# Performance work log

Hardware: AMD Instinct MI355X
Metric: run time of the kernel (lower is better)

## Reference

```python
import jax, jax.numpy as jnp
import numpy as np

B, K, L, D, H, A = 32, 512, 6, 2048, 16, 10
HD = D // H
OBS = 128
MAX_STEPS = 512


def _ln(x, g, b, eps=1e-5):
    m = x.mean(-1, keepdims=True)
    v = ((x - m) ** 2).mean(-1, keepdims=True)
    return (x - m) * jax.lax.rsqrt(v + eps) * g + b


def _pos_encoding(seq_len, dim):
    # torch: seq counts down from seq_len-1 to 0
    seq = jnp.arange(seq_len - 1, -1, -1, dtype=jnp.float32)
    inv = 10000.0 ** (-(jnp.arange(0, dim, 2, dtype=jnp.float32)) / dim)
    si = seq[:, None] * inv[None, :]
    return jnp.concatenate([jnp.sin(si), jnp.cos(si)], axis=-1)  # [seq_len, dim]


def setup_inputs() -> dict:
    key = jax.random.key(0)
    ks = jax.random.split(key, 16)
    s = 0.02
    inp = {}
    inp['x'] = jax.random.normal(ks[0], (B, OBS), jnp.float32)
    inp['memories'] = jax.random.normal(ks[1], (B, K, L, D), jnp.float32)
    inp['mask'] = jax.random.randint(ks[2], (B, K), 0, 2, jnp.int32)
    inp['memory_indices'] = jax.random.randint(ks[3], (B, K), 0, MAX_STEPS, jnp.int32)
    # encoder (vector-obs Linear)
    inp['enc_w'] = jax.random.normal(ks[4], (D, OBS), jnp.float32) * s
    inp['enc_b'] = jnp.zeros((D,), jnp.float32)
    # per-layer params, stacked on leading L axis
    inp['lnq_g'] = jnp.ones((L, D), jnp.float32)
    inp['lnq_b'] = jnp.zeros((L, D), jnp.float32)
    inp['lnkv_g'] = jnp.ones((L, D), jnp.float32)
    inp['lnkv_b'] = jnp.zeros((L, D), jnp.float32)
    inp['lnattn_g'] = jnp.ones((L, D), jnp.float32)
    inp['lnattn_b'] = jnp.zeros((L, D), jnp.float32)
    inp['wq'] = jax.random.normal(ks[5], (L, HD, HD), jnp.float32) * s
    inp['wk'] = jax.random.normal(ks[6], (L, HD, HD), jnp.float32) * s
    inp['wv'] = jax.random.normal(ks[7], (L, HD, HD), jnp.float32) * s
    inp['wo'] = jax.random.normal(ks[8], (L, D, D), jnp.float32) * s
    inp['bo'] = jnp.zeros((L, D), jnp.float32)
    inp['fc_w'] = jax.random.normal(ks[9], (L, D, D), jnp.float32) * s
    inp['fc_b'] = jnp.zeros((L, D), jnp.float32)
    # heads
    inp['post_w'] = jax.random.normal(ks[10], (D, D), jnp.float32) * s
    inp['post_b'] = jnp.zeros((D,), jnp.float32)
    inp['actor_w'] = jax.random.normal(ks[11], (A, D), jnp.float32) * 0.01
    inp['actor_b'] = jnp.zeros((A,), jnp.float32)
    inp['critic_w'] = jax.random.normal(ks[12], (1, D), jnp.float32) * s
    inp['critic_b'] = jnp.zeros((1,), jnp.float32)
    return inp


def reference(x, memories, mask, memory_indices, enc_w, enc_b,
              lnq_g, lnq_b, lnkv_g, lnkv_b, lnattn_g, lnattn_b,
              wq, wk, wv, wo, bo, fc_w, fc_b,
              post_w, post_b, actor_w, actor_b, critic_w, critic_b):
    h = x @ enc_w.T + enc_b                              # [B, D] encoder
    pe = _pos_encoding(MAX_STEPS, D)[memory_indices]      # [B, K, D]
    mems = memories + pe[:, :, None, :]                   # [B, K, L, D]
    mems_t = jnp.moveaxis(mems, 2, 0)                     # [L, B, K, D]
    maskf = mask[:, None, :] != 0                         # [B, 1, K] -> bcast over heads
    inv_scale = 1.0 / jnp.sqrt(jnp.float32(D))            # note: full embed_dim, as in source

    def body(xq, p):
        lg, lb, kg, kb, ag, ab, Wq, Wk, Wv, Wo, bo_, Fw, Fb, mem = p
        q_ = _ln(xq, lg, lb)                              # [B, D] (query LN)
        kv = _ln(mem, kg, kb)                             # [B, K, D] (key = value = LN(mem))
        q = jnp.einsum('bhd,ed->bhe', q_.reshape(B, H, HD), Wq)
        k = jnp.einsum('bkhd,ed->bkhe', kv.reshape(B, K, H, HD), Wk)
        v = jnp.einsum('bkhd,ed->bkhe', kv.reshape(B, K, H, HD), Wv)
        energy = jnp.einsum('bhd,bkhd->bhk', q, k)        # [B, H, K]
        energy = jnp.where(maskf, energy, jnp.float32(-1e20))
        attn = jax.nn.softmax(energy * inv_scale, axis=-1)
        o = jnp.einsum('bhk,bkhd->bhd', attn, v).reshape(B, D)
        o = o @ Wo.T + bo_                                # fc_out
        xr = o + xq                                       # residual
        f = jax.nn.relu(_ln(xr, ag, ab) @ Fw.T + Fb)      # LN + MLP
        return f + xr, None

    h, _ = jax.lax.scan(
        body, h,
        (lnq_g, lnq_b, lnkv_g, lnkv_b, lnattn_g, lnattn_b,
         wq, wk, wv, wo, bo, fc_w, fc_b, mems_t))

    hid = jax.nn.relu(h @ post_w.T + post_b)
    logits = hid @ actor_w.T + actor_b                    # [B, A]
    value = hid @ critic_w.T + critic_b                   # [B, 1]
    return jnp.concatenate([logits, value], axis=-1)      # [B, A+1]
```

## Files before the change

kernel.cpp:

```cpp
#include <hip/hip_runtime.h>
#include <math.h>

namespace {

constexpr int B_ = 32, K_ = 512, L_ = 6, D_ = 2048, H_ = 16, HD_ = 128;
constexpr int OBS_ = 128, MAXS_ = 512, A_ = 10;
constexpr int NCH = 64, WKEYS = 8;
constexpr int KSPLIT = 8, KCHUNK = 256;
constexpr float EPS = 1e-5f;
constexpr float INV_SCALE = 0.022097086912079608f;

__device__ __forceinline__ float wsum64(float v) {
  v += __shfl_xor(v, 32); v += __shfl_xor(v, 16); v += __shfl_xor(v, 8);
  v += __shfl_xor(v, 4);  v += __shfl_xor(v, 2);  v += __shfl_xor(v, 1);
  return v;
}

__global__ __launch_bounds__(256) void k_pe(float* __restrict__ pe) {
  int s = blockIdx.x, t = threadIdx.x;
  float seqv = (float)(MAXS_ - 1 - s);
  const float c = 13.287712379549449f / 1024.0f;
  for (int r = 0; r < 8; ++r) {
    int j = t + 256 * r;
    int i = (j < 1024) ? j : j - 1024;
    float inv = exp2f(-c * (float)i);
    float a = seqv * inv;
    pe[(size_t)s * D_ + j] = (j < 1024) ? sinf(a) : cosf(a);
  }
}

__global__ __launch_bounds__(128) void k_enc(const float* __restrict__ x,
                                             const float* __restrict__ ew,
                                             const float* __restrict__ eb,
                                             float* __restrict__ h) {
  int b = blockIdx.x, et = blockIdx.y, t = threadIdx.x;
  __shared__ float xs[OBS_];
  xs[t] = x[b * OBS_ + t];
  __syncthreads();
  int e = et * 128 + t;
  const float* wr = ew + (size_t)e * OBS_;
  float acc = eb[e];
  for (int o = 0; o < OBS_; ++o) acc += xs[o] * wr[o];
  h[(size_t)b * D_ + e] = acc;
}

__global__ __launch_bounds__(256) void k_qw(const float* __restrict__ h,
                                            const float* __restrict__ g,
                                            const float* __restrict__ bvec,
                                            const float* __restrict__ Wq,
                                            const float* __restrict__ Wk,
                                            float* __restrict__ qW) {
  int b = blockIdx.x, t = threadIdx.x;
  int lane = t & 63, wv = t >> 6;
  __shared__ float qn[D_];
  __shared__ float qs[D_];
  __shared__ float rs[4], rq[4];
  float4 v0 = *(const float4*)(h + (size_t)b * D_ + t * 8);
  float4 v1 = *(const float4*)(h + (size_t)b * D_ + t * 8 + 4);
  float ls = v0.x + v0.y + v0.z + v0.w + v1.x + v1.y + v1.z + v1.w;
  float lq = v0.x * v0.x + v0.y * v0.y + v0.z * v0.z + v0.w * v0.w +
             v1.x * v1.x + v1.y * v1.y + v1.z * v1.z + v1.w * v1.w;
  ls = wsum64(ls); lq = wsum64(lq);
  if (lane == 0) { rs[wv] = ls; rq[wv] = lq; }
  __syncthreads();
  float sum = rs[0] + rs[1] + rs[2] + rs[3];
  float sq  = rq[0] + rq[1] + rq[2] + rq[3];
  float mean = sum * (1.f / D_);
  float rstd = rsqrtf(sq * (1.f / D_) - mean * mean + EPS);
  {
    float4 g0 = *(const float4*)(g + t * 8);
    float4 g1 = *(const float4*)(g + t * 8 + 4);
    float4 b0 = *(const float4*)(bvec + t * 8);
    float4 b1 = *(const float4*)(bvec + t * 8 + 4);
    qn[t * 8 + 0] = (v0.x - mean) * rstd * g0.x + b0.x;
    qn[t * 8 + 1] = (v0.y - mean) * rstd * g0.y + b0.y;
    qn[t * 8 + 2] = (v0.z - mean) * rstd * g0.z + b0.z;
    qn[t * 8 + 3] = (v0.w - mean) * rstd * g0.w + b0.w;
    qn[t * 8 + 4] = (v1.x - mean) * rstd * g1.x + b1.x;
    qn[t * 8 + 5] = (v1.y - mean) * rstd * g1.y + b1.y;
    qn[t * 8 + 6] = (v1.z - mean) * rstd * g1.z + b1.z;
    qn[t * 8 + 7] = (v1.w - mean) * rstd * g1.w + b1.w;
  }
  __syncthreads();
  int qid = t >> 4;
  int li = t & 15;
  for (int e = 0; e < 128; ++e) {
    const float4* wr = (const float4*)(Wq + (size_t)e * HD_ + li * 8);
    const float4* qv = (const float4*)(qn + qid * HD_ + li * 8);
    float4 w0 = wr[0], w1 = wr[1], a0 = qv[0], a1 = qv[1];
    float acc = w0.x * a0.x + w0.y * a0.y + w0.z * a0.z + w0.w * a0.w +
                w1.x * a1.x + w1.y * a1.y + w1.z * a1.z + w1.w * a1.w;
    acc += __shfl_xor(acc, 1); acc += __shfl_xor(acc, 2);
    acc += __shfl_xor(acc, 4); acc += __shfl_xor(acc, 8);
    if (li == 0) qs[qid * HD_ + e] = acc;
  }
  __syncthreads();
  for (int r = 0; r < 8; ++r) {
    int j = t + 256 * r;
    int hh = j >> 7, d = j & 127;
    const float* qv = qs + hh * HD_;
    float acc = 0.f;
    for (int e = 0; e < HD_; ++e) acc += qv[e] * Wk[(size_t)e * HD_ + d];
    qW[(size_t)b * D_ + j] = acc * INV_SCALE;
  }
}

__global__ __launch_bounds__(256) void k_attn(const float* __restrict__ mem,
                                              const float* __restrict__ pe,
                                              const int* __restrict__ mask,
                                              const int* __restrict__ midx,
                                              const float* __restrict__ g,
                                              const float* __restrict__ bvec,
                                              const float* __restrict__ qW,
                                              float* __restrict__ pm,
                                              float* __restrict__ ps,
                                              float* __restrict__ pctx,
                                              int layer) {
  int b = blockIdx.x;
  int t = threadIdx.x;
  int wid = t >> 6, l = t & 63;
  int ch = blockIdx.y * 4 + wid;
  int hi = l >> 5;
  int ll = l & 31;

  __shared__ float gs[D_], bs[D_], qs[D_];
  for (int i = t; i < D_ / 4; i += 256) {
    ((float4*)gs)[i] = ((const float4*)g)[i];
    ((float4*)bs)[i] = ((const float4*)bvec)[i];
    ((float4*)qs)[i] = ((const float4*)(qW + (size_t)b * D_))[i];
  }
  __syncthreads();

  float m[8], s[8];
  float4 ctx[8];
  #pragma unroll
  for (int i = 0; i < 8; ++i) {
    m[i] = -INFINITY; s[i] = 0.f; ctx[i] = {0.f, 0.f, 0.f, 0.f};
  }

  const size_t browbase = ((size_t)b * K_) * (L_ * D_) + (size_t)layer * D_;
  int kk0 = ch * WKEYS;
  for (int kk = kk0; kk < kk0 + WKEYS; ++kk) {
    if (mask[b * K_ + kk] == 0) continue;
    int pidx = midx[b * K_ + kk];
    const float4* mp = (const float4*)(mem + browbase + (size_t)kk * (L_ * D_));
    const float4* pp = (const float4*)(pe + (size_t)pidx * D_);
    float4 x[8];
    #pragma unroll
    for (int i = 0; i < 8; ++i) {
      float4 a = mp[i * 64 + l];
      float4 c = pp[i * 64 + l];
      x[i] = {a.x + c.x, a.y + c.y, a.z + c.z, a.w + c.w};
    }
    float ls = 0.f, lq = 0.f;
    #pragma unroll
    for (int i = 0; i < 8; ++i) {
      ls += x[i].x + x[i].y + x[i].z + x[i].w;
      lq += x[i].x * x[i].x + x[i].y * x[i].y + x[i].z * x[i].z + x[i].w * x[i].w;
    }
    ls = wsum64(ls); lq = wsum64(lq);
    float mean = ls * (1.f / D_);
    float rstd = rsqrtf(lq * (1.f / D_) - mean * mean + EPS);
    #pragma unroll
    for (int i = 0; i < 8; ++i) {
      int idx = i * 64 + l;
      float4 g4 = ((const float4*)gs)[idx];
      float4 b4 = ((const float4*)bs)[idx];
      float4 q4 = ((const float4*)qs)[idx];
      float4 kv;
      kv.x = (x[i].x - mean) * rstd * g4.x + b4.x;
      kv.y = (x[i].y - mean) * rstd * g4.y + b4.y;
      kv.z = (x[i].z - mean) * rstd * g4.z + b4.z;
      kv.w = (x[i].w - mean) * rstd * g4.w + b4.w;
      float p = kv.x * q4.x + kv.y * q4.y + kv.z * q4.z + kv.w * q4.w;
      p += __shfl_xor(p, 1); p += __shfl_xor(p, 2); p += __shfl_xor(p, 4);
      p += __shfl_xor(p, 8); p += __shfl_xor(p, 16);
      float mn = fmaxf(m[i], p);
      float sc = __expf(m[i] - mn);
      float w = __expf(p - mn);
      s[i] = s[i] * sc + w;
      ctx[i].x = ctx[i].x * sc + w * kv.x;
      ctx[i].y = ctx[i].y * sc + w * kv.y;
      ctx[i].z = ctx[i].z * sc + w * kv.z;
      ctx[i].w = ctx[i].w * sc + w * kv.w;
      m[i] = mn;
    }
  }

  #pragma unroll
  for (int i = 0; i < 8; ++i) {
    int head = 2 * i + hi;
    size_t base = (size_t)(b * H_ + head) * NCH + ch;
    *(float4*)(pctx + base * HD_ + 4 * ll) = ctx[i];
    if (ll == 0) { pm[base] = m[i]; ps[base] = s[i]; }
  }
}

__global__ __launch_bounds__(128) void k_reduce(const float* __restrict__ pm,
                                                const float* __restrict__ ps,
                                                const float* __restrict__ pctx,
                                                const float* __restrict__ Wv,
                                                float* __restrict__ opre) {
  int hh = blockIdx.x, b = blockIdx.y;
  int t = threadIdx.x;
  size_t base = (size_t)(b * H_ + hh) * NCH;
  float m = -INFINITY;
  for (int c = 0; c < NCH; ++c) m = fmaxf(m, pm[base + c]);
  float stot = 0.f, acc = 0.f;
  for (int c = 0; c < NCH; ++c) {
    float wc = __expf(pm[base + c] - m);
    stot += ps[base + c] * wc;
    acc += pctx[(base + c) * HD_ + t] * wc;
  }
  float ctxn = (stot > 0.f) ? acc / stot : 0.f;
  __shared__ float cs[HD_];
  cs[t] = ctxn;
  __syncthreads();
  const float* wr = Wv + (size_t)t * HD_;
  float o = 0.f;
  for (int d = 0; d < HD_; ++d) o += wr[d] * cs[d];
  opre[(size_t)b * D_ + hh * HD_ + t] = o;
}

__global__ __launch_bounds__(256) void k_mv(const float* __restrict__ X,
                                            const float* __restrict__ W,
                                            float* __restrict__ part) {
  int et = blockIdx.x, kc = blockIdx.y;
  int t = threadIdx.x;
  __shared__ float xs[32][260];
  for (int r = 0; r < 8; ++r) {
    int i = t + 256 * r;
    int b = i >> 6, j = i & 63;
    float4 v = *(const float4*)(X + (size_t)b * D_ + kc * KCHUNK + 4 * j);
    *(float4*)(&xs[b][4 * j]) = v;
  }
  __syncthreads();
  int b = t & 31, eg = t >> 5;
  const float* wbase = W + (size_t)(et * 64 + eg * 8) * D_ + kc * KCHUNK;
  float acc[8] = {0.f, 0.f, 0.f, 0.f, 0.f, 0.f, 0.f, 0.f};
  for (int j = 0; j < 64; ++j) {
    float4 x4 = *(const float4*)(&xs[b][4 * j]);
    #pragma unroll
    for (int i = 0; i < 8; ++i) {
      float4 w4 = *(const float4*)(wbase + (size_t)i * D_ + 4 * j);
      acc[i] += w4.x * x4.x + w4.y * x4.y + w4.z * x4.z + w4.w * x4.w;
    }
  }
  float* pb = part + ((size_t)b * KSPLIT + kc) * D_ + et * 64 + eg * 8;
  float4 o0 = {acc[0], acc[1], acc[2], acc[3]};
  float4 o1 = {acc[4], acc[5], acc[6], acc[7]};
  *(float4*)pb = o0;
  *(float4*)(pb + 4) = o1;
}

__global__ __launch_bounds__(256) void k_mvred_ln(const float* __restrict__ part,
                                                  const float* __restrict__ bias,
                                                  const float* __restrict__ res,
                                                  const float* __restrict__ g,
                                                  const float* __restrict__ bvec,
                                                  float* __restrict__ xr,
                                                  float* __restrict__ xn) {
  int b = blockIdx.x, t = threadIdx.x;
  int lane = t & 63, wv = t >> 6;
  __shared__ float rs[4], rq[4];
  float4 v[2];
  float ls = 0.f, lq = 0.f;
  #pragma unroll
  for (int r = 0; r < 2; ++r) {
    int e4 = t + 256 * r;
    float4 a = {0.f, 0.f, 0.f, 0.f};
    for (int kc = 0; kc < KSPLIT; ++kc) {
      float4 p = ((const float4*)(part + ((size_t)b * KSPLIT + kc) * D_))[e4];
      a.x += p.x; a.y += p.y; a.z += p.z; a.w += p.w;
    }
    float4 b4 = ((const float4*)bias)[e4];
    float4 h4 = ((const float4*)(res + (size_t)b * D_))[e4];
    a.x += b4.x + h4.x; a.y += b4.y + h4.y; a.z += b4.z + h4.z; a.w += b4.w + h4.w;
    v[r] = a;
    ls += a.x + a.y + a.z + a.w;
    lq += a.x * a.x + a.y * a.y + a.z * a.z + a.w * a.w;
  }
  ls = wsum64(ls); lq = wsum64(lq);
  if (lane == 0) { rs[wv] = ls; rq[wv] = lq; }
  __syncthreads();
  float sum = rs[0] + rs[1] + rs[2] + rs[3];
  float sq  = rq[0] + rq[1] + rq[2] + rq[3];
  float mean = sum * (1.f / D_);
  float rstd = rsqrtf(sq * (1.f / D_) - mean * mean + EPS);
  #pragma unroll
  for (int r = 0; r < 2; ++r) {
    int e4 = t + 256 * r;
    float4 a = v[r];
    ((float4*)(xr + (size_t)b * D_))[e4] = a;
    float4 g4 = ((const float4*)g)[e4];
    float4 b4 = ((const float4*)bvec)[e4];
    float4 n;
    n.x = (a.x - mean) * rstd * g4.x + b4.x;
    n.y = (a.y - mean) * rstd * g4.y + b4.y;
    n.z = (a.z - mean) * rstd * g4.z + b4.z;
    n.w = (a.w - mean) * rstd * g4.w + b4.w;
    ((float4*)(xn + (size_t)b * D_))[e4] = n;
  }
}

__global__ __launch_bounds__(256) void k_mvred_relu(const float* __restrict__ part,
                                                    const float* __restrict__ bias,
                                                    const float* __restrict__ res,
                                                    float* __restrict__ out) {
  int b = blockIdx.x, t = threadIdx.x;
  #pragma unroll
  for (int r = 0; r < 2; ++r) {
    int e4 = t + 256 * r;
    float4 a = {0.f, 0.f, 0.f, 0.f};
    for (int kc = 0; kc < KSPLIT; ++kc) {
      float4 p = ((const float4*)(part + ((size_t)b * KSPLIT + kc) * D_))[e4];
      a.x += p.x; a.y += p.y; a.z += p.z; a.w += p.w;
    }
    float4 b4 = ((const float4*)bias)[e4];
    a.x = fmaxf(a.x + b4.x, 0.f); a.y = fmaxf(a.y + b4.y, 0.f);
    a.z = fmaxf(a.z + b4.z, 0.f); a.w = fmaxf(a.w + b4.w, 0.f);
    if (res) {
      float4 h4 = ((const float4*)(res + (size_t)b * D_))[e4];
      a.x += h4.x; a.y += h4.y; a.z += h4.z; a.w += h4.w;
    }
    ((float4*)(out + (size_t)b * D_))[e4] = a;
  }
}

__global__ __launch_bounds__(256) void k_heads(const float* __restrict__ hid,
                                               const float* __restrict__ aw,
                                               const float* __restrict__ ab,
                                               const float* __restrict__ cw,
                                               const float* __restrict__ cb,
                                               float* __restrict__ out) {
  int b = blockIdx.x, j = blockIdx.y;
  int t = threadIdx.x, lane = t & 63, wv = t >> 6;
  const float* wr = (j < A_) ? (aw + (size_t)j * D_) : cw;
  float acc = 0.f;
  for (int i = t; i < D_ / 4; i += 256) {
    float4 w = ((const float4*)wr)[i];
    float4 xv = ((const float4*)(hid + (size_t)b * D_))[i];
    acc += w.x * xv.x + w.y * xv.y + w.z * xv.z + w.w * xv.w;
  }
  acc = wsum64(acc);
  __shared__ float r[4];
  if (lane == 0) r[wv] = acc;
  __syncthreads();
  if (t == 0) {
    float s = r[0] + r[1] + r[2] + r[3] + ((j < A_) ? ab[j] : cb[0]);
    out[b * (A_ + 1) + j] = s;
  }
}

}

extern "C" void kernel_launch(void* const* d_in, const int* in_sizes, int n_in,
                              void* d_out, int out_size, void* d_ws, size_t ws_size,
                              hipStream_t stream) {
  (void)in_sizes; (void)n_in; (void)out_size; (void)ws_size;
  const float* x      = (const float*)d_in[0];
  const float* mem    = (const float*)d_in[1];
  const int*   mask   = (const int*)d_in[2];
  const int*   midx   = (const int*)d_in[3];
  const float* enc_w  = (const float*)d_in[4];
  const float* enc_b  = (const float*)d_in[5];
  const float* lnq_g  = (const float*)d_in[6];
  const float* lnq_b  = (const float*)d_in[7];
  const float* lnkv_g = (const float*)d_in[8];
  const float* lnkv_b = (const float*)d_in[9];
  const float* lnat_g = (const float*)d_in[10];
  const float* lnat_b = (const float*)d_in[11];
  const float* wq     = (const float*)d_in[12];
  const float* wk     = (const float*)d_in[13];
  const float* wv     = (const float*)d_in[14];
  const float* wo     = (const float*)d_in[15];
  const float* bo     = (const float*)d_in[16];
  const float* fc_w   = (const float*)d_in[17];
  const float* fc_b   = (const float*)d_in[18];
  const float* post_w = (const float*)d_in[19];
  const float* post_b = (const float*)d_in[20];
  const float* act_w  = (const float*)d_in[21];
  const float* act_b  = (const float*)d_in[22];
  const float* cri_w  = (const float*)d_in[23];
  const float* cri_b  = (const float*)d_in[24];
  float* out = (float*)d_out;

  float* ws = (float*)d_ws;
  size_t off = 0;
  float* pe   = ws + off; off += (size_t)MAXS_ * D_;
  float* h    = ws + off; off += (size_t)B_ * D_;
  float* qW   = ws + off; off += (size_t)B_ * D_;
  float* opre = ws + off; off += (size_t)B_ * D_;
  float* xr   = ws + off; off += (size_t)B_ * D_;
  float* xn   = ws + off; off += (size_t)B_ * D_;
  float* hid  = ws + off; off += (size_t)B_ * D_;
  float* pm   = ws + off; off += (size_t)B_ * H_ * NCH;
  float* ps   = ws + off; off += (size_t)B_ * H_ * NCH;
  float* pctx = ws + off; off += (size_t)B_ * H_ * NCH * HD_;
  float* part = ws + off; off += (size_t)B_ * KSPLIT * D_;

  hipLaunchKernelGGL(k_pe, dim3(MAXS_), dim3(256), 0, stream, pe);
  hipLaunchKernelGGL(k_enc, dim3(B_, D_ / 128), dim3(128), 0, stream, x, enc_w, enc_b, h);

  for (int l = 0; l < L_; ++l) {
    const float* Wq = wq + (size_t)l * HD_ * HD_;
    const float* Wk = wk + (size_t)l * HD_ * HD_;
    const float* Wv = wv + (size_t)l * HD_ * HD_;
    const float* Wo = wo + (size_t)l * D_ * D_;
    const float* Fw = fc_w + (size_t)l * D_ * D_;
    hipLaunchKernelGGL(k_qw, dim3(B_), dim3(256), 0, stream,
                       h, lnq_g + (size_t)l * D_, lnq_b + (size_t)l * D_, Wq, Wk, qW);
    hipLaunchKernelGGL(k_attn, dim3(B_, NCH / 4), dim3(256), 0, stream,
                       mem, pe, mask, midx,
                       lnkv_g + (size_t)l * D_, lnkv_b + (size_t)l * D_,
                       qW, pm, ps, pctx, l);
    hipLaunchKernelGGL(k_reduce, dim3(H_, B_), dim3(128), 0, stream,
                       pm, ps, pctx, Wv, opre);
    hipLaunchKernelGGL(k_mv, dim3(D_ / 64, KSPLIT), dim3(256), 0, stream, opre, Wo, part);
    hipLaunchKernelGGL(k_mvred_ln, dim3(B_), dim3(256), 0, stream,
                       part, bo + (size_t)l * D_, h,
                       lnat_g + (size_t)l * D_, lnat_b + (size_t)l * D_, xr, xn);
    hipLaunchKernelGGL(k_mv, dim3(D_ / 64, KSPLIT), dim3(256), 0, stream, xn, Fw, part);
    hipLaunchKernelGGL(k_mvred_relu, dim3(B_), dim3(256), 0, stream,
                       part, fc_b + (size_t)l * D_, xr, h);
  }

  hipLaunchKernelGGL(k_mv, dim3(D_ / 64, KSPLIT), dim3(256), 0, stream, h, post_w, part);
  hipLaunchKernelGGL(k_mvred_relu, dim3(B_), dim3(256), 0, stream,
                     part, post_b, (const float*)nullptr, hid);
  hipLaunchKernelGGL(k_heads, dim3(B_, A_ + 1), dim3(256), 0, stream,
                     hid, act_w, act_b, cri_w, cri_b, out);
}
```

Before: 1.077 ms.

## Fuse whole forward pass into one persistent cooperative kernel with grid syncs

```diff
diff --git a/kernel.cpp b/kernel.cpp
--- a/kernel.cpp
+++ b/kernel.cpp
@@ -1,5 +1,8 @@
 #include <hip/hip_runtime.h>
+#include <hip/hip_cooperative_groups.h>
 #include <math.h>
+
+namespace cg = cooperative_groups;
 
 namespace {
 
@@ -7,14 +10,388 @@
 constexpr int OBS_ = 128, MAXS_ = 512, A_ = 10;
 constexpr int NCH = 64, WKEYS = 8;
 constexpr int KSPLIT = 8, KCHUNK = 256;
+constexpr int NBLK = 256, NTHR = 512;
 constexpr float EPS = 1e-5f;
 constexpr float INV_SCALE = 0.022097086912079608f;
+
+struct Params {
+  const float *x, *mem;
+  const int *mask, *midx;
+  const float *enc_w, *enc_b;
+  const float *lnq_g, *lnq_b, *lnkv_g, *lnkv_b, *lnat_g, *lnat_b;
+  const float *wq, *wk, *wv, *wo, *bo, *fc_w, *fc_b;
+  const float *post_w, *post_b, *act_w, *act_b, *cri_w, *cri_b;
+  float *out;
+  float *pe, *h, *qW, *opre, *xr, *xn, *hid, *pm, *ps, *pctx, *part;
+};
 
 __device__ __forceinline__ float wsum64(float v) {
   v += __shfl_xor(v, 32); v += __shfl_xor(v, 16); v += __shfl_xor(v, 8);
   v += __shfl_xor(v, 4);  v += __shfl_xor(v, 2);  v += __shfl_xor(v, 1);
   return v;
 }
+
+
+__global__ __launch_bounds__(NTHR, 2) void k_fused(Params P) {
+  cg::grid_group grid = cg::this_grid();
+  const int g = blockIdx.x, t = threadIdx.x;
+  const int lane = t & 63, wv = t >> 6;
+  __shared__ float smem[8320];
+
+  {
+    int b = g >> 3, ec = g & 7;
+    if (t < 32) ((float4*)smem)[t] = ((const float4*)(P.x + b * OBS_))[t];
+    int half = t >> 8, tt = t & 255;
+    int s = g + 256 * half;
+    float seqv = (float)(MAXS_ - 1 - s);
+    const float c = 13.287712379549449f / 1024.0f;
+    #pragma unroll
+    for (int r = 0; r < 8; ++r) {
+      int j = tt + 256 * r;
+      int i = (j < 1024) ? j : j - 1024;
+      float inv = exp2f(-c * (float)i);
+      float a = seqv * inv;
+      P.pe[(size_t)s * D_ + j] = (j < 1024) ? sinf(a) : cosf(a);
+    }
+    __syncthreads();
+    if (t < 256) {
+      int e = ec * 256 + t;
+      const float* wr = P.enc_w + (size_t)e * OBS_;
+      float acc = 0.f;
+      #pragma unroll
+      for (int o = 0; o < OBS_; o += 4) {
+        float4 w = *(const float4*)(wr + o);
+        acc += w.x * smem[o] + w.y * smem[o + 1] + w.z * smem[o + 2] + w.w * smem[o + 3];
+      }
+      P.h[(size_t)b * D_ + e] = acc + P.enc_b[e];
+    }
+  }
+  grid.sync();
+
+  for (int l = 0; l < L_; ++l) {
+    const float* Wq = P.wq + (size_t)l * HD_ * HD_;
+    const float* Wk = P.wk + (size_t)l * HD_ * HD_;
+    const float* Wv = P.wv + (size_t)l * HD_ * HD_;
+    const float* Wo = P.wo + (size_t)l * D_ * D_;
+    const float* Fw = P.fc_w + (size_t)l * D_ * D_;
+    const float* qg = P.lnq_g + (size_t)l * D_,  *qb = P.lnq_b + (size_t)l * D_;
+    const float* kg = P.lnkv_g + (size_t)l * D_, *kb = P.lnkv_b + (size_t)l * D_;
+    const float* ag = P.lnat_g + (size_t)l * D_, *ab = P.lnat_b + (size_t)l * D_;
+    const float* bo_ = P.bo + (size_t)l * D_;
+    const float* fb = P.fc_b + (size_t)l * D_;
+
+    if (g < B_) {
+      int b = g;
+      float* qn = smem;
+      float* qs2 = smem + 2048;
+      float* rs = smem + 4096; float* rq = smem + 4104;
+      float4 v0 = *(const float4*)(P.h + (size_t)b * D_ + t * 4);
+      float ls = v0.x + v0.y + v0.z + v0.w;
+      float lq = v0.x * v0.x + v0.y * v0.y + v0.z * v0.z + v0.w * v0.w;
+      ls = wsum64(ls); lq = wsum64(lq);
+      if (lane == 0) { rs[wv] = ls; rq[wv] = lq; }
+      __syncthreads();
+      float sum = 0.f, sq = 0.f;
+      #pragma unroll
+      for (int w = 0; w < 8; ++w) { sum += rs[w]; sq += rq[w]; }
+      float mean = sum * (1.f / D_);
+      float rstd = rsqrtf(sq * (1.f / D_) - mean * mean + EPS);
+      {
+        float4 g0 = *(const float4*)(qg + t * 4);
+        float4 b0 = *(const float4*)(qb + t * 4);
+        qn[t * 4 + 0] = (v0.x - mean) * rstd * g0.x + b0.x;
+        qn[t * 4 + 1] = (v0.y - mean) * rstd * g0.y + b0.y;
+        qn[t * 4 + 2] = (v0.z - mean) * rstd * g0.z + b0.z;
+        qn[t * 4 + 3] = (v0.w - mean) * rstd * g0.w + b0.w;
+      }
+      __syncthreads();
+      int qid = t >> 5, li = t & 31;
+      for (int e = 0; e < 128; ++e) {
+        float4 w0 = *(const float4*)(Wq + (size_t)e * HD_ + li * 4);
+        float4 a0 = *(const float4*)(qn + qid * HD_ + li * 4);
+        float acc = w0.x * a0.x + w0.y * a0.y + w0.z * a0.z + w0.w * a0.w;
+        acc += __shfl_xor(acc, 1); acc += __shfl_xor(acc, 2);
+        acc += __shfl_xor(acc, 4); acc += __shfl_xor(acc, 8);
+        acc += __shfl_xor(acc, 16);
+        if (li == 0) qs2[qid * HD_ + e] = acc;
+      }
+      __syncthreads();
+      #pragma unroll
+      for (int r = 0; r < 4; ++r) {
+        int j = t + 512 * r;
+        int hh = j >> 7, d = j & 127;
+        const float* qv = qs2 + hh * HD_;
+        float acc = 0.f;
+        for (int e = 0; e < HD_; ++e) acc += qv[e] * Wk[(size_t)e * HD_ + d];
+        P.qW[(size_t)b * D_ + j] = acc * INV_SCALE;
+      }
+    }
+    grid.sync();
+
+    {
+      int b = g >> 3;
+      int wid = t >> 6, l64 = t & 63;
+      int ch = (g & 7) * 8 + wid;
+      int hi = l64 >> 5, ll = l64 & 31;
+      float* gs = smem; float* bs = smem + 2048; float* qs = smem + 4096;
+      for (int i = t; i < D_ / 4; i += NTHR) {
+        ((float4*)gs)[i] = ((const float4*)kg)[i];
+        ((float4*)bs)[i] = ((const float4*)kb)[i];
+        ((float4*)qs)[i] = ((const float4*)(P.qW + (size_t)b * D_))[i];
+      }
+      __syncthreads();
+      float m[8], s[8];
+      float4 ctx[8];
+      #pragma unroll
+      for (int i = 0; i < 8; ++i) {
+        m[i] = -INFINITY; s[i] = 0.f; ctx[i] = {0.f, 0.f, 0.f, 0.f};
+      }
+      const size_t browbase = ((size_t)b * K_) * (L_ * D_) + (size_t)l * D_;
+      int kk0 = ch * WKEYS;
+      for (int kk = kk0; kk < kk0 + WKEYS; ++kk) {
+        if (P.mask[b * K_ + kk] == 0) continue;
+        int pidx = P.midx[b * K_ + kk];
+        const float4* mp = (const float4*)(P.mem + browbase + (size_t)kk * (L_ * D_));
+        const float4* pp = (const float4*)(P.pe + (size_t)pidx * D_);
+        float4 xv[8];
+        #pragma unroll
+        for (int i = 0; i < 8; ++i) {
+          float4 a = mp[i * 64 + l64];
+          float4 c = pp[i * 64 + l64];
+          xv[i] = {a.x + c.x, a.y + c.y, a.z + c.z, a.w + c.w};
+        }
+        float ls = 0.f, lq = 0.f;
+        #pragma unroll
+        for (int i = 0; i < 8; ++i) {
+          ls += xv[i].x + xv[i].y + xv[i].z + xv[i].w;
+          lq += xv[i].x * xv[i].x + xv[i].y * xv[i].y + xv[i].z * xv[i].z + xv[i].w * xv[i].w;
+        }
+        ls = wsum64(ls); lq = wsum64(lq);
+        float mean = ls * (1.f / D_);
+        float rstd = rsqrtf(lq * (1.f / D_) - mean * mean + EPS);
+        #pragma unroll
+        for (int i = 0; i < 8; ++i) {
+          int idx = i * 64 + l64;
+          float4 g4 = ((const float4*)gs)[idx];
+          float4 b4 = ((const float4*)bs)[idx];
+          float4 q4 = ((const float4*)qs)[idx];
+          float4 kv;
+          kv.x = (xv[i].x - mean) * rstd * g4.x + b4.x;
+          kv.y = (xv[i].y - mean) * rstd * g4.y + b4.y;
+          kv.z = (xv[i].z - mean) * rstd * g4.z + b4.z;
+          kv.w = (xv[i].w - mean) * rstd * g4.w + b4.w;
+          float p = kv.x * q4.x + kv.y * q4.y + kv.z * q4.z + kv.w * q4.w;
+          p += __shfl_xor(p, 1); p += __shfl_xor(p, 2); p += __shfl_xor(p, 4);
+          p += __shfl_xor(p, 8); p += __shfl_xor(p, 16);
+          float mn = fmaxf(m[i], p);
+          float sc = __expf(m[i] - mn);
+          float w = __expf(p - mn);
+          s[i] = s[i] * sc + w;
+          ctx[i].x = ctx[i].x * sc + w * kv.x;
+          ctx[i].y = ctx[i].y * sc + w * kv.y;
+          ctx[i].z = ctx[i].z * sc + w * kv.z;
+          ctx[i].w = ctx[i].w * sc + w * kv.w;
+          m[i] = mn;
+        }
+      }
+      #pragma unroll
+      for (int i = 0; i < 8; ++i) {
+        int head = 2 * i + hi;
+        size_t base = (size_t)(b * H_ + head) * NCH + ch;
+        *(float4*)(P.pctx + base * HD_ + 4 * ll) = ctx[i];
+        if (ll == 0) { P.pm[base] = m[i]; P.ps[base] = s[i]; }
+      }
+    }
+    grid.sync();
+
+    {
+      int b = g >> 3;
+      int hh = (g & 7) * 2 + (t >> 8);
+      int tt = t & 255;
+      float* cs = smem + (t >> 8) * 128;
+      if (tt < 128) {
+        size_t base = (size_t)(b * H_ + hh) * NCH;
+        float m = -INFINITY;
+        for (int c = 0; c < NCH; ++c) m = fmaxf(m, P.pm[base + c]);
+        float stot = 0.f, acc = 0.f;
+        for (int c = 0; c < NCH; ++c) {
+          float wc = __expf(P.pm[base + c] - m);
+          stot += P.ps[base + c] * wc;
+          acc += P.pctx[(base + c) * HD_ + tt] * wc;
+        }
+        cs[tt] = (stot > 0.f) ? acc / stot : 0.f;
+      }
+      __syncthreads();
+      if (tt < 128) {
+        const float* wr = Wv + (size_t)tt * HD_;
+        float o = 0.f;
+        for (int d = 0; d < HD_; ++d) o += wr[d] * cs[d];
+        P.opre[(size_t)b * D_ + hh * HD_ + tt] = o;
+      }
+    }
+    grid.sync();
+
+    {
+      int et = g >> 3, kc = g & 7;
+      float (*xs)[260] = (float (*)[260])smem;
+      #pragma unroll
+      for (int r = 0; r < 4; ++r) {
+        int fi = (r * NTHR + t) * 4;
+        int b = fi >> 8, k0 = fi & 255;
+        *(float4*)&xs[b][k0] = *(const float4*)(P.opre + (size_t)b * D_ + kc * KCHUNK + k0);
+      }
+      __syncthreads();
+      int b = t & 31, eg = t >> 5;
+      const float* wbase = Wo + (size_t)(et * 64 + eg * 4) * D_ + kc * KCHUNK;
+      float acc[4] = {0.f, 0.f, 0.f, 0.f};
+      for (int j = 0; j < KCHUNK / 4; ++j) {
+        float4 x4 = *(const float4*)&xs[b][4 * j];
+        #pragma unroll
+        for (int i = 0; i < 4; ++i) {
+          float4 w4 = *(const float4*)(wbase + (size_t)i * D_ + 4 * j);
+          acc[i] += w4.x * x4.x + w4.y * x4.y + w4.z * x4.z + w4.w * x4.w;
+        }
+      }
+      float4 o0 = {acc[0], acc[1], acc[2], acc[3]};
+      *(float4*)(P.part + ((size_t)b * KSPLIT + kc) * D_ + et * 64 + eg * 4) = o0;
+      __syncthreads();
+    }
+    grid.sync();
+    if (g < B_) {
+      int b = g;
+      float* rs = smem; float* rq = smem + 8;
+      float4 a = {0.f, 0.f, 0.f, 0.f};
+      for (int kc = 0; kc < KSPLIT; ++kc) {
+        float4 p = ((const float4*)(P.part + ((size_t)b * KSPLIT + kc) * D_))[t];
+        a.x += p.x; a.y += p.y; a.z += p.z; a.w += p.w;
+      }
+      float4 b4 = ((const float4*)bo_)[t];
+      float4 h4 = ((const float4*)(P.h + (size_t)b * D_))[t];
+      a.x += b4.x + h4.x; a.y += b4.y + h4.y; a.z += b4.z + h4.z; a.w += b4.w + h4.w;
+      float ls = a.x + a.y + a.z + a.w;
+      float lq = a.x * a.x + a.y * a.y + a.z * a.z + a.w * a.w;
+      ls = wsum64(ls); lq = wsum64(lq);
+      if (lane == 0) { rs[wv] = ls; rq[wv] = lq; }
+      __syncthreads();
+      float sum = 0.f, sq = 0.f;
+      #pragma unroll
+      for (int w = 0; w < 8; ++w) { sum += rs[w]; sq += rq[w]; }
+      float mean = sum * (1.f / D_);
+      float rstd = rsqrtf(sq * (1.f / D_) - mean * mean + EPS);
+      ((float4*)(P.xr + (size_t)b * D_))[t] = a;
+      float4 g4 = ((const float4*)ag)[t];
+      float4 bb = ((const float4*)ab)[t];
+      float4 n;
+      n.x = (a.x - mean) * rstd * g4.x + bb.x;
+      n.y = (a.y - mean) * rstd * g4.y + bb.y;
+      n.z = (a.z - mean) * rstd * g4.z + bb.z;
+      n.w = (a.w - mean) * rstd * g4.w + bb.w;
+      ((float4*)(P.xn + (size_t)b * D_))[t] = n;
+    }
+    grid.sync();
+
+    {
+      int et = g >> 3, kc = g & 7;
+      float (*xs)[260] = (float (*)[260])smem;
+      #pragma unroll
+      for (int r = 0; r < 4; ++r) {
+        int fi = (r * NTHR + t) * 4;
+        int b = fi >> 8, k0 = fi & 255;
+        *(float4*)&xs[b][k0] = *(const float4*)(P.xn + (size_t)b * D_ + kc * KCHUNK + k0);
+      }
+      __syncthreads();
+      int b = t & 31, eg = t >> 5;
+      const float* wbase = Fw + (size_t)(et * 64 + eg * 4) * D_ + kc * KCHUNK;
+      float acc[4] = {0.f, 0.f, 0.f, 0.f};
+      for (int j = 0; j < KCHUNK / 4; ++j) {
+        float4 x4 = *(const float4*)&xs[b][4 * j];
+        #pragma unroll
+        for (int i = 0; i < 4; ++i) {
+          float4 w4 = *(const float4*)(wbase + (size_t)i * D_ + 4 * j);
+          acc[i] += w4.x * x4.x + w4.y * x4.y + w4.z * x4.z + w4.w * x4.w;
+        }
+      }
+      float4 o0 = {acc[0], acc[1], acc[2], acc[3]};
+      *(float4*)(P.part + ((size_t)b * KSPLIT + kc) * D_ + et * 64 + eg * 4) = o0;
+      __syncthreads();
+    }
+    grid.sync();
+    if (g < B_) {
+      int b = g;
+      float4 a = {0.f, 0.f, 0.f, 0.f};
+      for (int kc = 0; kc < KSPLIT; ++kc) {
+        float4 p = ((const float4*)(P.part + ((size_t)b * KSPLIT + kc) * D_))[t];
+        a.x += p.x; a.y += p.y; a.z += p.z; a.w += p.w;
+      }
+      float4 b4 = ((const float4*)fb)[t];
+      a.x = fmaxf(a.x + b4.x, 0.f); a.y = fmaxf(a.y + b4.y, 0.f);
+      a.z = fmaxf(a.z + b4.z, 0.f); a.w = fmaxf(a.w + b4.w, 0.f);
+      float4 h4 = ((const float4*)(P.xr + (size_t)b * D_))[t];
+      a.x += h4.x; a.y += h4.y; a.z += h4.z; a.w += h4.w;
+      ((float4*)(P.h + (size_t)b * D_))[t] = a;
+    }
+    grid.sync();
+  }
+
+  {
+    int et = g >> 3, kc = g & 7;
+    float (*xs)[260] = (float (*)[260])smem;
+    #pragma unroll
+    for (int r = 0; r < 4; ++r) {
+      int fi = (r * NTHR + t) * 4;
+      int b = fi >> 8, k0 = fi & 255;
+      *(float4*)&xs[b][k0] = *(const float4*)(P.h + (size_t)b * D_ + kc * KCHUNK + k0);
+    }
+    __syncthreads();
+    int b = t & 31, eg = t >> 5;
+    const float* wbase = P.post_w + (size_t)(et * 64 + eg * 4) * D_ + kc * KCHUNK;
+    float acc[4] = {0.f, 0.f, 0.f, 0.f};
+    for (int j = 0; j < KCHUNK / 4; ++j) {
+      float4 x4 = *(const float4*)&xs[b][4 * j];
+      #pragma unroll
+      for (int i = 0; i < 4; ++i) {
+        float4 w4 = *(const float4*)(wbase + (size_t)i * D_ + 4 * j);
+        acc[i] += w4.x * x4.x + w4.y * x4.y + w4.z * x4.z + w4.w * x4.w;
+      }
+    }
+    float4 o0 = {acc[0], acc[1], acc[2], acc[3]};
+    *(float4*)(P.part + ((size_t)b * KSPLIT + kc) * D_ + et * 64 + eg * 4) = o0;
+    __syncthreads();
+  }
+  grid.sync();
+  if (g < B_) {
+    int b = g;
+    float4 a = {0.f, 0.f, 0.f, 0.f};
+    for (int kc = 0; kc < KSPLIT; ++kc) {
+      float4 p = ((const float4*)(P.part + ((size_t)b * KSPLIT + kc) * D_))[t];
+      a.x += p.x; a.y += p.y; a.z += p.z; a.w += p.w;
+    }
+    float4 b4 = ((const float4*)P.post_b)[t];
+    a.x = fmaxf(a.x + b4.x, 0.f); a.y = fmaxf(a.y + b4.y, 0.f);
+    a.z = fmaxf(a.z + b4.z, 0.f); a.w = fmaxf(a.w + b4.w, 0.f);
+    ((float4*)(P.hid + (size_t)b * D_))[t] = a;
+  }
+  grid.sync();
+  if (g < B_) {
+    int b = g;
+    ((float4*)smem)[t] = ((const float4*)(P.hid + (size_t)b * D_))[t];
+    __syncthreads();
+    int w = t >> 6;
+    for (int j = w; j < A_ + 1; j += 8) {
+      const float* wr = (j < A_) ? (P.act_w + (size_t)j * D_) : P.cri_w;
+      float acc = 0.f;
+      for (int i = lane; i < D_ / 4; i += 64) {
+        float4 wv4 = ((const float4*)wr)[i];
+        float4 xv = ((const float4*)smem)[i];
+        acc += wv4.x * xv.x + wv4.y * xv.y + wv4.z * xv.z + wv4.w * xv.w;
+      }
+      acc = wsum64(acc);
+      if (lane == 0)
+        P.out[b * (A_ + 1) + j] = acc + ((j < A_) ? P.act_b[j] : P.cri_b[0]);
+    }
+  }
+}
+
 
 __global__ __launch_bounds__(256) void k_pe(float* __restrict__ pe) {
   int s = blockIdx.x, t = threadIdx.x;
@@ -82,8 +459,7 @@
     qn[t * 8 + 7] = (v1.w - mean) * rstd * g1.w + b1.w;
   }
   __syncthreads();
-  int qid = t >> 4;
-  int li = t & 15;
+  int qid = t >> 4, li = t & 15;
   for (int e = 0; e < 128; ++e) {
     const float4* wr = (const float4*)(Wq + (size_t)e * HD_ + li * 8);
     const float4* qv = (const float4*)(qn + qid * HD_ + li * 8);
@@ -120,9 +496,7 @@
   int t = threadIdx.x;
   int wid = t >> 6, l = t & 63;
   int ch = blockIdx.y * 4 + wid;
-  int hi = l >> 5;
-  int ll = l & 31;
-
+  int hi = l >> 5, ll = l & 31;
   __shared__ float gs[D_], bs[D_], qs[D_];
   for (int i = t; i < D_ / 4; i += 256) {
     ((float4*)gs)[i] = ((const float4*)g)[i];
@@ -130,14 +504,12 @@
     ((float4*)qs)[i] = ((const float4*)(qW + (size_t)b * D_))[i];
   }
   __syncthreads();
-
   float m[8], s[8];
   float4 ctx[8];
   #pragma unroll
   for (int i = 0; i < 8; ++i) {
     m[i] = -INFINITY; s[i] = 0.f; ctx[i] = {0.f, 0.f, 0.f, 0.f};
   }
-
   const size_t browbase = ((size_t)b * K_) * (L_ * D_) + (size_t)layer * D_;
   int kk0 = ch * WKEYS;
   for (int kk = kk0; kk < kk0 + WKEYS; ++kk) {
@@ -145,18 +517,18 @@
     int pidx = midx[b * K_ + kk];
     const float4* mp = (const float4*)(mem + browbase + (size_t)kk * (L_ * D_));
     const float4* pp = (const float4*)(pe + (size_t)pidx * D_);
-    float4 x[8];
+    float4 xv[8];
     #pragma unroll
     for (int i = 0; i < 8; ++i) {
       float4 a = mp[i * 64 + l];
       float4 c = pp[i * 64 + l];
-      x[i] = {a.x + c.x, a.y + c.y, a.z + c.z, a.w + c.w};
+      xv[i] = {a.x + c.x, a.y + c.y, a.z + c.z, a.w + c.w};
     }
     float ls = 0.f, lq = 0.f;
     #pragma unroll
     for (int i = 0; i < 8; ++i) {
-      ls += x[i].x + x[i].y + x[i].z + x[i].w;
-      lq += x[i].x * x[i].x + x[i].y * x[i].y + x[i].z * x[i].z + x[i].w * x[i].w;
+      ls += xv[i].x + xv[i].y + xv[i].z + xv[i].w;
+      lq += xv[i].x * xv[i].x + xv[i].y * xv[i].y + xv[i].z * xv[i].z + xv[i].w * xv[i].w;
     }
     ls = wsum64(ls); lq = wsum64(lq);
     float mean = ls * (1.f / D_);
@@ -168,10 +540,10 @@
       float4 b4 = ((const float4*)bs)[idx];
       float4 q4 = ((const float4*)qs)[idx];
       float4 kv;
-      kv.x = (x[i].x - mean) * rstd * g4.x + b4.x;
-      kv.y = (x[i].y - mean) * rstd * g4.y + b4.y;
-      kv.z = (x[i].z - mean) * rstd * g4.z + b4.z;
-      kv.w = (x[i].w - mean) * rstd * g4.w + b4.w;
+      kv.x = (xv[i].x - mean) * rstd * g4.x + b4.x;
+      kv.y = (xv[i].y - mean) * rstd * g4.y + b4.y;
+      kv.z = (xv[i].z - mean) * rstd * g4.z + b4.z;
+      kv.w = (xv[i].w - mean) * rstd * g4.w + b4.w;
       float p = kv.x * q4.x + kv.y * q4.y + kv.z * q4.z + kv.w * q4.w;
       p += __shfl_xor(p, 1); p += __shfl_xor(p, 2); p += __shfl_xor(p, 4);
       p += __shfl_xor(p, 8); p += __shfl_xor(p, 16);
@@ -186,7 +558,6 @@
       m[i] = mn;
     }
   }
-
   #pragma unroll
   for (int i = 0; i < 8; ++i) {
     int head = 2 * i + hi;
@@ -358,76 +729,97 @@
                               void* d_out, int out_size, void* d_ws, size_t ws_size,
                               hipStream_t stream) {
   (void)in_sizes; (void)n_in; (void)out_size; (void)ws_size;
-  const float* x      = (const float*)d_in[0];
-  const float* mem    = (const float*)d_in[1];
-  const int*   mask   = (const int*)d_in[2];
-  const int*   midx   = (const int*)d_in[3];
-  const float* enc_w  = (const float*)d_in[4];
-  const float* enc_b  = (const float*)d_in[5];
-  const float* lnq_g  = (const float*)d_in[6];
-  const float* lnq_b  = (const float*)d_in[7];
-  const float* lnkv_g = (const float*)d_in[8];
-  const float* lnkv_b = (const float*)d_in[9];
-  const float* lnat_g = (const float*)d_in[10];
-  const float* lnat_b = (const float*)d_in[11];
-  const float* wq     = (const float*)d_in[12];
-  const float* wk     = (const float*)d_in[13];
-  const float* wv     = (const float*)d_in[14];
-  const float* wo     = (const float*)d_in[15];
-  const float* bo     = (const float*)d_in[16];
-  const float* fc_w   = (const float*)d_in[17];
-  const float* fc_b   = (const float*)d_in[18];
-  const float* post_w = (const float*)d_in[19];
-  const float* post_b = (const float*)d_in[20];
-  const float* act_w  = (const float*)d_in[21];
-  const float* act_b  = (const float*)d_in[22];
-  const float* cri_w  = (const float*)d_in[23];
-  const float* cri_b  = (const float*)d_in[24];
-  float* out = (float*)d_out;
+  Params p;
+  p.x      = (const float*)d_in[0];
+  p.mem    = (const float*)d_in[1];
+  p.mask   = (const int*)d_in[2];
+  p.midx   = (const int*)d_in[3];
+  p.enc_w  = (const float*)d_in[4];
+  p.enc_b  = (const float*)d_in[5];
+  p.lnq_g  = (const float*)d_in[6];
+  p.lnq_b  = (const float*)d_in[7];
+  p.lnkv_g = (const float*)d_in[8];
+  p.lnkv_b = (const float*)d_in[9];
+  p.lnat_g = (const float*)d_in[10];
+  p.lnat_b = (const float*)d_in[11];
+  p.wq     = (const float*)d_in[12];
+  p.wk     = (const float*)d_in[13];
+  p.wv     = (const float*)d_in[14];
+  p.wo     = (const float*)d_in[15];
+  p.bo     = (const float*)d_in[16];
+  p.fc_w   = (const float*)d_in[17];
+  p.fc_b   = (const float*)d_in[18];
+  p.post_w = (const float*)d_in[19];
+  p.post_b = (const float*)d_in[20];
+  p.act_w  = (const float*)d_in[21];
+  p.act_b  = (const float*)d_in[22];
+  p.cri_w  = (const float*)d_in[23];
+  p.cri_b  = (const float*)d_in[24];
+  p.out    = (float*)d_out;
 
   float* ws = (float*)d_ws;
   size_t off = 0;
-  float* pe   = ws + off; off += (size_t)MAXS_ * D_;
-  float* h    = ws + off; off += (size_t)B_ * D_;
-  float* qW   = ws + off; off += (size_t)B_ * D_;
-  float* opre = ws + off; off += (size_t)B_ * D_;
-  float* xr   = ws + off; off += (size_t)B_ * D_;
-  float* xn   = ws + off; off += (size_t)B_ * D_;
-  float* hid  = ws + off; off += (size_t)B_ * D_;
-  float* pm   = ws + off; off += (size_t)B_ * H_ * NCH;
-  float* ps   = ws + off; off += (size_t)B_ * H_ * NCH;
-  float* pctx = ws + off; off += (size_t)B_ * H_ * NCH * HD_;
-  float* part = ws + off; off += (size_t)B_ * KSPLIT * D_;
-
-  hipLaunchKernelGGL(k_pe, dim3(MAXS_), dim3(256), 0, stream, pe);
-  hipLaunchKernelGGL(k_enc, dim3(B_, D_ / 128), dim3(128), 0, stream, x, enc_w, enc_b, h);
-
+  p.pe   = ws + off; off += (size_t)MAXS_ * D_;
+  p.h    = ws + off; off += (size_t)B_ * D_;
+  p.qW   = ws + off; off += (size_t)B_ * D_;
+  p.opre = ws + off; off += (size_t)B_ * D_;
+  p.xr   = ws + off; off += (size_t)B_ * D_;
+  p.xn   = ws + off; off += (size_t)B_ * D_;
+  p.hid  = ws + off; off += (size_t)B_ * D_;
+  p.pm   = ws + off; off += (size_t)B_ * H_ * NCH;
+  p.ps   = ws + off; off += (size_t)B_ * H_ * NCH;
+  p.pctx = ws + off; off += (size_t)B_ * H_ * NCH * HD_;
+  p.part = ws + off; off += (size_t)B_ * KSPLIT * D_;
+
+  bool use_coop = false;
+  {
+    int dev = 0;
+    (void)hipGetDevice(&dev);
+    int coop = 0;
+    (void)hipDeviceGetAttribute(&coop, hipDeviceAttributeCooperativeLaunch, dev);
+    int ncu = 0;
+    (void)hipDeviceGetAttribute(&ncu, hipDeviceAttributeMultiprocessorCount, dev);
+    int maxb = 0;
+    (void)hipOccupancyMaxActiveBlocksPerMultiprocessor(&maxb, k_fused, NTHR, 0);
+    use_coop = (coop != 0) && ((long)maxb * (long)ncu >= (long)NBLK);
+  }
+
+  if (use_coop) {
+    void* args[] = {&p};
+    hipError_t e = hipLaunchCooperativeKernel(k_fused, dim3(NBLK), dim3(NTHR),
+                                              args, 0, stream);
+    if (e == hipSuccess) return;
+    (void)hipGetLastError();
+  }
+
+  hipLaunchKernelGGL(k_pe, dim3(MAXS_), dim3(256), 0, stream, p.pe);
+  hipLaunchKernelGGL(k_enc, dim3(B_, D_ / 128), dim3(128), 0, stream,
+                     p.x, p.enc_w, p.enc_b, p.h);
   for (int l = 0; l < L_; ++l) {
-    const float* Wq = wq + (size_t)l * HD_ * HD_;
-    const float* Wk = wk + (size_t)l * HD_ * HD_;
-    const float* Wv = wv + (size_t)l * HD_ * HD_;
-    const float* Wo = wo + (size_t)l * D_ * D_;
-    const float* Fw = fc_w + (size_t)l * D_ * D_;
+    const float* Wq = p.wq + (size_t)l * HD_ * HD_;
+    const float* Wk = p.wk + (size_t)l * HD_ * HD_;
+    const float* Wv = p.wv + (size_t)l * HD_ * HD_;
+    const float* Wo = p.wo + (size_t)l * D_ * D_;
+    const float* Fw = p.fc_w + (size_t)l * D_ * D_;
     hipLaunchKernelGGL(k_qw, dim3(B_), dim3(256), 0, stream,
-                       h, lnq_g + (size_t)l * D_, lnq_b + (size_t)l * D_, Wq, Wk, qW);
+                       p.h, p.lnq_g + (size_t)l * D_, p.lnq_b + (size_t)l * D_, Wq, Wk, p.qW);
     hipLaunchKernelGGL(k_attn, dim3(B_, NCH / 4), dim3(256), 0, stream,
-                       mem, pe, mask, midx,
-                       lnkv_g + (size_t)l * D_, lnkv_b + (size_t)l * D_,
-                       qW, pm, ps, pctx, l);
+                       p.mem, p.pe, p.mask, p.midx,
+                       p.lnkv_g + (size_t)l * D_, p.lnkv_b + (size_t)l * D_,
+                       p.qW, p.pm, p.ps, p.pctx, l);
     hipLaunchKernelGGL(k_reduce, dim3(H_, B_), dim3(128), 0, stream,
-                       pm, ps, pctx, Wv, opre);
-    hipLaunchKernelGGL(k_mv, dim3(D_ / 64, KSPLIT), dim3(256), 0, stream, opre, Wo, part);
+                       p.pm, p.ps, p.pctx, Wv, p.opre);
+    hipLaunchKernelGGL(k_mv, dim3(D_ / 64, KSPLIT), dim3(256), 0, stream, p.opre, Wo, p.part);
     hipLaunchKernelGGL(k_mvred_ln, dim3(B_), dim3(256), 0, stream,
-                       part, bo + (size_t)l * D_, h,
-                       lnat_g + (size_t)l * D_, lnat_b + (size_t)l * D_, xr, xn);
-    hipLaunchKernelGGL(k_mv, dim3(D_ / 64, KSPLIT), dim3(256), 0, stream, xn, Fw, part);
+                       p.part, p.bo + (size_t)l * D_, p.h,
+                       p.lnat_g + (size_t)l * D_, p.lnat_b + (size_t)l * D_, p.xr, p.xn);
+    hipLaunchKernelGGL(k_mv, dim3(D_ / 64, KSPLIT), dim3(256), 0, stream, p.xn, Fw, p.part);
     hipLaunchKernelGGL(k_mvred_relu, dim3(B_), dim3(256), 0, stream,
-                       part, fc_b + (size_t)l * D_, xr, h);
-  }
-
-  hipLaunchKernelGGL(k_mv, dim3(D_ / 64, KSPLIT), dim3(256), 0, stream, h, post_w, part);
+                       p.part, p.fc_b + (size_t)l * D_, p.xr, p.h);
+  }
+  hipLaunchKernelGGL(k_mv, dim3(D_ / 64, KSPLIT), dim3(256), 0, stream, p.h, p.post_w, p.part);
   hipLaunchKernelGGL(k_mvred_relu, dim3(B_), dim3(256), 0, stream,
-                     part, post_b, (const float*)nullptr, hid);
+                     p.part, p.post_b, (const float*)nullptr, p.hid);
   hipLaunchKernelGGL(k_heads, dim3(B_, A_ + 1), dim3(256), 0, stream,
-                     hid, act_w, act_b, cri_w, cri_b, out);
-}
+                     p.hid, p.act_w, p.act_b, p.cri_w, p.cri_b, p.out);
+}
```

Measured after the change: 1.079 ms. About the same (+0.2%).
